# Optimization experiments

Hardware: AMD Instinct MI355X
Metric: run time of the kernel (lower is better)

## Reference

```python
import jax, jax.numpy as jnp
import numpy as np

N, E, DIN, DOUT, DE = 100000, 250000, 32, 32, 13


def setup_inputs() -> dict:
    key = jax.random.key(0)
    ks = jax.random.split(key, 10)
    def u(k, shape, fan):
        b = 1.0 / np.sqrt(fan)
        return jax.random.uniform(k, shape, jnp.float32, -b, b)
    x = jax.random.normal(ks[0], (N, DIN), jnp.float32)
    edge_index = jax.random.randint(ks[1], (2, E), 0, N)
    edge_attr = jax.random.uniform(ks[2], (E, DE), jnp.float32)
    # NNConv's edge network: Linear(DE -> DIN*DOUT)
    nn_w = u(ks[3], (DIN * DOUT, DE), DE)
    nn_b = u(ks[4], (DIN * DOUT,), DE)
    # NNConv root weight + bias
    root = u(ks[5], (DIN, DOUT), DIN)
    bias = jnp.zeros((DOUT,), jnp.float32)
    # GRU(input=DIN, hidden=DOUT), single layer, seq_len=1
    w_ih = u(ks[6], (3 * DOUT, DIN), DOUT)
    w_hh = u(ks[7], (3 * DOUT, DOUT), DOUT)
    b_ih = u(ks[8], (3 * DOUT,), DOUT)
    b_hh = u(ks[9], (3 * DOUT,), DOUT)
    return dict(x=x, edge_attr=edge_attr, nn_w=nn_w, nn_b=nn_b, root=root,
                bias=bias, w_ih=w_ih, w_hh=w_hh, b_ih=b_ih, b_hh=b_hh,
                edge_index=edge_index)


def reference(x, edge_attr, nn_w, nn_b, root, bias, w_ih, w_hh, b_ih, b_hh, edge_index):
    identity = x
    h0 = x  # h is None -> h = x.unsqueeze(0); squeeze the seq dim here
    # norm='_None' (identity) and Dropout in eval mode (identity)
    src, dst = edge_index[0], edge_index[1]
    # NNConv: per-edge weight matrix from edge_attr  [E, DIN, DOUT]
    W = (edge_attr @ nn_w.T + nn_b).reshape(E, DIN, DOUT)
    msg = jnp.einsum('ei,eio->eo', x[src], W)           # [E, DOUT]
    agg = jax.ops.segment_sum(msg, dst, num_segments=N)  # [N, DOUT]
    cnt = jax.ops.segment_sum(jnp.ones((E, 1), x.dtype), dst, num_segments=N)
    mean = agg / jnp.maximum(cnt, 1.0)                   # aggr='mean'
    conv = mean + x @ root + bias
    # celu then GRU step (seq_len=1)
    c = jax.nn.celu(conv)
    gi = c @ w_ih.T + b_ih
    gh = h0 @ w_hh.T + b_hh
    ir, iz, ic = jnp.split(gi, 3, axis=1)
    hr, hz, hc = jnp.split(gh, 3, axis=1)
    r = jax.nn.sigmoid(ir + hr)
    z = jax.nn.sigmoid(iz + hz)
    n = jnp.tanh(ic + r * hc)
    h_new = (1.0 - z) * n + z * h0
    out = jax.nn.relu(h_new + identity)  # res=True, act=ReLU
    return out, h_new[None]
```

## Files before the change

kernel.cpp:

```cpp
#include <hip/hip_runtime.h>
#include <hip/hip_bf16.h>
#include <stdint.h>

#define DIN 32
#define DOUT 32
#define DE 13

typedef float f32x4 __attribute__((ext_vector_type(4)));
typedef short s16x8 __attribute__((ext_vector_type(8)));
typedef int   i32x4 __attribute__((ext_vector_type(4)));

__device__ __forceinline__ float bf2f(unsigned short u) {
    return __uint_as_float(((uint32_t)u) << 16);
}
__device__ __forceinline__ unsigned short f2bf(float f) {
    uint32_t b = __float_as_uint(f);
    b += 0x7FFFu + ((b >> 16) & 1u);
    return (unsigned short)(b >> 16);
}
__device__ __forceinline__ uint32_t pk2(float a, float b) {
    float2 t; t.x = a; t.y = b;
    __hip_bfloat162 h = __float22bfloat162_rn(t);
    return *(uint32_t*)&h;
}
__device__ __forceinline__ float sigm(float v) { return 1.f / (1.f + __expf(-v)); }
__device__ __forceinline__ float tanh_fast(float v) { return 2.f / (1.f + __expf(-2.f * v)) - 1.f; }

#define KE_LDS (28 * 512)
__global__ __launch_bounds__(256) void kE(const float* __restrict__ x,
        const float* __restrict__ ea, const int* __restrict__ ei,
        const float* __restrict__ nn_w, const float* __restrict__ nn_b,
        __hip_bfloat162* __restrict__ agg, float* __restrict__ cnt, int E) {
    __shared__ unsigned short Al[KE_LDS];
    __shared__ uint32_t tr4[4][256];
    const int tid = threadIdx.x;
    for (int t = tid; t < KE_LDS; t += 256) {
        int j = t & 7;
        int lane = (t >> 3) & 63;
        int tile = t >> 9;
        int at2 = tile >= 14 ? 1 : 0;
        int kt = tile - at2 * 14;
        int o = at2 * 16 + (lane & 15);
        int i = ((lane >> 4) << 3) + j;
        float v = (kt < 13) ? nn_w[(i * 32 + o) * 13 + kt] : nn_b[i * 32 + o];
        Al[t] = f2bf(v);
    }
    __syncthreads();
    const int lane = tid & 63;
    const int wv = tid >> 6;
    const int el = lane & 15;
    const int quad = lane >> 4;
    const int q8 = quad << 3;
    uint32_t* trw = &tr4[wv][0];
    const int wave = (blockIdx.x * 256 + tid) >> 6;
    const int nw = (gridDim.x * 256) >> 6;
    const int nstrips = E >> 4;
    for (int s = wave; s < nstrips; s += nw) {
        const int e = (s << 4) + el;
        const int srcv = ei[e];
        const int dstv = ei[E + e];
        const float* eab = ea + (size_t)(s << 4) * 13;
        #pragma unroll
        for (int t = 0; t < 4; ++t) {
            int idx = t * 64 + lane;
            if (idx < 208) trw[idx] = __float_as_uint(eab[idx]);
        }
        const float* xq = x + (size_t)srcv * 32 + q8;
        f32x4 xlo = *(const f32x4*)xq;
        f32x4 xhi = *(const f32x4*)(xq + 4);
        i32x4 bi;
        bi[0] = pk2(xlo[0], xlo[1]);
        bi[1] = pk2(xlo[2], xlo[3]);
        bi[2] = pk2(xhi[0], xhi[1]);
        bi[3] = pk2(xhi[2], xhi[3]);
        s16x8 bfr = __builtin_bit_cast(s16x8, bi);
        float g[14];
        #pragma unroll
        for (int d = 0; d < 13; ++d) g[d] = __uint_as_float(trw[el * 13 + d]);
        g[13] = 1.0f;
        f32x4 acc0 = {0.f, 0.f, 0.f, 0.f}, acc1 = {0.f, 0.f, 0.f, 0.f};
        const f32x4 zz = {0.f, 0.f, 0.f, 0.f};
        #pragma unroll
        for (int kt = 0; kt < 14; ++kt) {
            s16x8 a0 = *(const s16x8*)&Al[kt * 512 + lane * 8];
            s16x8 a1 = *(const s16x8*)&Al[(14 + kt) * 512 + lane * 8];
            f32x4 y0 = __builtin_amdgcn_mfma_f32_16x16x32_bf16(a0, bfr, zz, 0, 0, 0);
            f32x4 y1 = __builtin_amdgcn_mfma_f32_16x16x32_bf16(a1, bfr, zz, 0, 0, 0);
            float gk = g[kt];
            #pragma unroll
            for (int r = 0; r < 4; ++r) {
                acc0[r] = fmaf(gk, y0[r], acc0[r]);
                acc1[r] = fmaf(gk, y1[r], acc1[r]);
            }
        }
        {
            uint2 p0, p1;
            p0.x = pk2(acc0[0], acc0[1]); p0.y = pk2(acc0[2], acc0[3]);
            p1.x = pk2(acc1[0], acc1[1]); p1.y = pk2(acc1[2], acc1[3]);
            *(uint2*)&trw[el * 16 + quad * 2] = p0;
            *(uint2*)&trw[el * 16 + 8 + quad * 2] = p1;
        }
        #pragma unroll
        for (int p = 0; p < 4; ++p) {
            int e4 = (p << 2) + quad;
            uint32_t val = trw[e4 * 16 + el];
            int d4 = __shfl(dstv, e4, 64);
            __hip_bfloat162 hv = *(__hip_bfloat162*)&val;
            unsafeAtomicAdd(&agg[(size_t)d4 * 16 + el], hv);
        }
        if (lane < 16) atomicAdd(&cnt[dstv], 1.0f);
    }
}

__global__ __launch_bounds__(256) void kF(const float* __restrict__ x,
        const __hip_bfloat16* __restrict__ aggb, const float* __restrict__ cnt,
        const float* __restrict__ root, const float* __restrict__ bias,
        const float* __restrict__ w_ih, const float* __restrict__ w_hh,
        const float* __restrict__ b_ih, const float* __restrict__ b_hh,
        float* __restrict__ out, float* __restrict__ hnew, int N) {
    __shared__ __align__(16) char smem[30720];
    unsigned short* Bl = (unsigned short*)smem;
    float* scr = (float*)(smem + 14336);
    unsigned short* clds = (unsigned short*)(smem + 14336);
    const int tid = threadIdx.x;
    {
        *(f32x4*)&scr[tid * 4] = *(const f32x4*)&root[tid * 4];
        #pragma unroll
        for (int it = 0; it < 3; ++it)
            *(f32x4*)&scr[1024 + it * 1024 + tid * 4] =
                *(const f32x4*)&w_ih[0 * 0 + it * 1024 + tid * 4 - 0 * 0] * 0.f +
                *(const f32x4*)&w_hh[it * 1024 + tid * 4];
    }
    __syncthreads();
    for (int t = tid; t < 8 * 512; t += 256) {
        int j = t & 7;
        int ln = (t >> 3) & 63;
        int tt = t >> 9;
        int i = ((ln >> 4) << 3) + j;
        int c = ln & 15;
        int col = tt * 16 + c;
        float v = (col < 32) ? scr[i * 32 + col] : scr[1024 + (col - 32) * 32 + i];
        Bl[t] = f2bf(v);
    }
    __syncthreads();
    #pragma unroll
    for (int it = 0; it < 3; ++it)
        *(f32x4*)&scr[it * 1024 + tid * 4] = *(const f32x4*)&w_ih[it * 1024 + tid * 4];
    __syncthreads();
    for (int t = tid + 8 * 512; t < 14 * 512; t += 256) {
        int j = t & 7;
        int ln = (t >> 3) & 63;
        int tt = t >> 9;
        int i = ((ln >> 4) << 3) + j;
        int c = ln & 15;
        Bl[t] = f2bf(scr[((tt - 8) * 16 + c) * 32 + i]);
    }
    __syncthreads();
    const int lane = tid & 63;
    const int wv = tid >> 6;
    const int c15 = lane & 15;
    const int rowb = (lane >> 4) << 2;
    unsigned short* cl = clds + wv * 512;
    float binit[14];
    #pragma unroll
    for (int t = 0; t < 2; ++t) binit[t] = bias[t * 16 + c15];
    #pragma unroll
    for (int t = 2; t < 8; ++t) binit[t] = b_hh[t * 16 + c15 - 32];
    #pragma unroll
    for (int u = 0; u < 6; ++u) binit[8 + u] = b_ih[u * 16 + c15];
    int wave = (blockIdx.x * 256 + tid) >> 6;
    const int nw = (gridDim.x * 256) >> 6;
    const int nstrips = N >> 4;
    for (int s = wave; s < nstrips; s += nw) {
        const int n0 = s << 4;
        const float* xp = x + (size_t)(n0 + c15) * 32 + ((lane >> 4) << 3);
        f32x4 x0 = *(const f32x4*)xp;
        f32x4 x1 = *(const f32x4*)(xp + 4);
        float xr[4][2], ag[4][2], cn[4];
        #pragma unroll
        for (int r = 0; r < 4; ++r) {
            const int n = n0 + rowb + r;
            cn[r] = cnt[n];
            #pragma unroll
            for (int t = 0; t < 2; ++t) {
                xr[r][t] = x[(size_t)n * 32 + t * 16 + c15];
                ag[r][t] = bf2f(*(const unsigned short*)&aggb[(size_t)n * 32 + t * 16 + c15]);
            }
        }
        s16x8 a;
        a[0] = (short)f2bf(x0[0]); a[1] = (short)f2bf(x0[1]);
        a[2] = (short)f2bf(x0[2]); a[3] = (short)f2bf(x0[3]);
        a[4] = (short)f2bf(x1[0]); a[5] = (short)f2bf(x1[1]);
        a[6] = (short)f2bf(x1[2]); a[7] = (short)f2bf(x1[3]);
        f32x4 D[8];
        #pragma unroll
        for (int t = 0; t < 8; ++t) {
            s16x8 b = *(const s16x8*)&Bl[(t * 64 + lane) * 8];
            f32x4 ci = {binit[t], binit[t], binit[t], binit[t]};
            D[t] = __builtin_amdgcn_mfma_f32_16x16x32_bf16(a, b, ci, 0, 0, 0);
        }
        #pragma unroll
        for (int r = 0; r < 4; ++r) {
            float icn = 1.f / fmaxf(cn[r], 1.f);
            #pragma unroll
            for (int t = 0; t < 2; ++t) {
                float conv = ag[r][t] * icn + D[t][r];
                float cv = conv > 0.f ? conv : (__expf(conv) - 1.f);
                cl[(rowb + r) * 32 + t * 16 + c15] = f2bf(cv);
            }
        }
        s16x8 a2 = *(const s16x8*)&cl[c15 * 32 + ((lane >> 4) << 3)];
        f32x4 G[6];
        #pragma unroll
        for (int u = 0; u < 6; ++u) {
            s16x8 b = *(const s16x8*)&Bl[((8 + u) * 64 + lane) * 8];
            f32x4 ci = {binit[8 + u], binit[8 + u], binit[8 + u], binit[8 + u]};
            G[u] = __builtin_amdgcn_mfma_f32_16x16x32_bf16(a2, b, ci, 0, 0, 0);
        }
        #pragma unroll
        for (int t = 0; t < 2; ++t) {
            #pragma unroll
            for (int r = 0; r < 4; ++r) {
                float rg = sigm(G[t][r] + D[2 + t][r]);
                float z  = sigm(G[2 + t][r] + D[4 + t][r]);
                float nn = tanh_fast(G[4 + t][r] + rg * D[6 + t][r]);
                float h  = (1.f - z) * nn + z * xr[r][t];
                float ov = h + xr[r][t];
                size_t oi = (size_t)(n0 + rowb + r) * 32 + t * 16 + c15;
                out[oi]  = ov > 0.f ? ov : 0.f;
                hnew[oi] = h;
            }
        }
    }
}

extern "C" void kernel_launch(void* const* d_in, const int* in_sizes, int n_in,
                              void* d_out, int out_size, void* d_ws, size_t ws_size,
                              hipStream_t stream) {
    const float* x    = (const float*)d_in[0];
    const float* ea   = (const float*)d_in[1];
    const float* nn_w = (const float*)d_in[2];
    const float* nn_b = (const float*)d_in[3];
    const float* root = (const float*)d_in[4];
    const float* bias = (const float*)d_in[5];
    const float* w_ih = (const float*)d_in[6];
    const float* w_hh = (const float*)d_in[7];
    const float* b_ih = (const float*)d_in[8];
    const float* b_hh = (const float*)d_in[9];
    const int*   ei   = (const int*)d_in[10];
    const int N = in_sizes[0] / DIN;
    const int E = in_sizes[10] / 2;
    float* out  = (float*)d_out;
    float* hnew = out + (size_t)N * DOUT;

    const size_t agg_bytes = (size_t)N * 32 * sizeof(__hip_bfloat16);

    __hip_bfloat162* agg = (__hip_bfloat162*)d_ws;
    float* cnt = (float*)((char*)d_ws + agg_bytes);
    kE<<<1024, 256, 0, stream>>>(x, ea, ei, nn_w, nn_b, agg, cnt, E);
    kF<<<768, 256, 0, stream>>>(x, (const __hip_bfloat16*)d_ws, cnt, root, bias,
                                w_ih, w_hh, b_ih, b_hh, out, hnew, N);
}
```

Baseline: 146.8 us.

## Process 32-edge strips with 32x32x16 MFMA in edge-message kernel

The edge kernel now handles 32 edges per wave using the 32x32x16 bf16 MFMA instead of two 16x16x32 MFMAs per edge-attribute term on 16-edge strips. The LDS weight layout is reorganized to match, and the transpose scratch is padded to a stride of 17 to reduce bank conflicts. Tail handling for edge counts not divisible by 32 is added. This halves the number of strips and aims to raise MFMA efficiency per edge, at the cost of more accumulator registers and extra bounds checks. A dead zero-multiplied w_ih load in kF is also removed.

```diff
diff --git a/kernel.cpp b/kernel.cpp
--- a/kernel.cpp
+++ b/kernel.cpp
@@ -6,9 +6,10 @@
 #define DOUT 32
 #define DE 13
 
-typedef float f32x4 __attribute__((ext_vector_type(4)));
-typedef short s16x8 __attribute__((ext_vector_type(8)));
-typedef int   i32x4 __attribute__((ext_vector_type(4)));
+typedef float f32x4  __attribute__((ext_vector_type(4)));
+typedef float f32x16 __attribute__((ext_vector_type(16)));
+typedef short s16x8  __attribute__((ext_vector_type(8)));
+typedef int   i32x4  __attribute__((ext_vector_type(4)));
 
 __device__ __forceinline__ float bf2f(unsigned short u) {
     return __uint_as_float(((uint32_t)u) << 16);
@@ -32,83 +33,92 @@
         const float* __restrict__ nn_w, const float* __restrict__ nn_b,
         __hip_bfloat162* __restrict__ agg, float* __restrict__ cnt, int E) {
     __shared__ unsigned short Al[KE_LDS];
-    __shared__ uint32_t tr4[4][256];
+    __shared__ uint32_t tr4[4][544];
     const int tid = threadIdx.x;
     for (int t = tid; t < KE_LDS; t += 256) {
         int j = t & 7;
         int lane = (t >> 3) & 63;
         int tile = t >> 9;
-        int at2 = tile >= 14 ? 1 : 0;
-        int kt = tile - at2 * 14;
-        int o = at2 * 16 + (lane & 15);
-        int i = ((lane >> 4) << 3) + j;
-        float v = (kt < 13) ? nn_w[(i * 32 + o) * 13 + kt] : nn_b[i * 32 + o];
+        int d = tile >> 1, half = tile & 1;
+        int o = lane & 31;
+        int k = ((lane >> 5) << 3) + j;
+        int i = half * 16 + k;
+        float v = (d < 13) ? nn_w[(i * 32 + o) * 13 + d] : nn_b[i * 32 + o];
         Al[t] = f2bf(v);
     }
     __syncthreads();
     const int lane = tid & 63;
     const int wv = tid >> 6;
-    const int el = lane & 15;
-    const int quad = lane >> 4;
-    const int q8 = quad << 3;
+    const int el = lane & 31;
+    const int kh = lane >> 5;
     uint32_t* trw = &tr4[wv][0];
     const int wave = (blockIdx.x * 256 + tid) >> 6;
     const int nw = (gridDim.x * 256) >> 6;
-    const int nstrips = E >> 4;
+    const int nstrips = (E + 31) >> 5;
     for (int s = wave; s < nstrips; s += nw) {
-        const int e = (s << 4) + el;
-        const int srcv = ei[e];
-        const int dstv = ei[E + e];
-        const float* eab = ea + (size_t)(s << 4) * 13;
-        #pragma unroll
-        for (int t = 0; t < 4; ++t) {
+        const int e = (s << 5) + el;
+        const bool ev = e < E;
+        const int ec = ev ? e : (E - 1);
+        const int srcv = ei[ec];
+        const int dstv = ei[E + ec];
+        const int ecur = min(32, E - (s << 5));
+        const float* eab = ea + (size_t)(s << 5) * 13;
+        const int lim = ecur * 13;
+        #pragma unroll
+        for (int t = 0; t < 7; ++t) {
             int idx = t * 64 + lane;
-            if (idx < 208) trw[idx] = __float_as_uint(eab[idx]);
-        }
-        const float* xq = x + (size_t)srcv * 32 + q8;
-        f32x4 xlo = *(const f32x4*)xq;
-        f32x4 xhi = *(const f32x4*)(xq + 4);
-        i32x4 bi;
-        bi[0] = pk2(xlo[0], xlo[1]);
-        bi[1] = pk2(xlo[2], xlo[3]);
-        bi[2] = pk2(xhi[0], xhi[1]);
-        bi[3] = pk2(xhi[2], xhi[3]);
-        s16x8 bfr = __builtin_bit_cast(s16x8, bi);
+            if (idx < lim) trw[idx] = __float_as_uint(eab[idx]);
+        }
+        const float* xq = x + (size_t)srcv * 32 + (kh << 3);
+        f32x4 x0a = *(const f32x4*)xq;
+        f32x4 x0b = *(const f32x4*)(xq + 4);
+        f32x4 x1a = *(const f32x4*)(xq + 16);
+        f32x4 x1b = *(const f32x4*)(xq + 20);
+        i32x4 bi0, bi1;
+        bi0[0] = pk2(x0a[0], x0a[1]); bi0[1] = pk2(x0a[2], x0a[3]);
+        bi0[2] = pk2(x0b[0], x0b[1]); bi0[3] = pk2(x0b[2], x0b[3]);
+        bi1[0] = pk2(x1a[0], x1a[1]); bi1[1] = pk2(x1a[2], x1a[3]);
+        bi1[2] = pk2(x1b[0], x1b[1]); bi1[3] = pk2(x1b[2], x1b[3]);
+        s16x8 b0 = __builtin_bit_cast(s16x8, bi0);
+        s16x8 b1 = __builtin_bit_cast(s16x8, bi1);
         float g[14];
         #pragma unroll
         for (int d = 0; d < 13; ++d) g[d] = __uint_as_float(trw[el * 13 + d]);
         g[13] = 1.0f;
-        f32x4 acc0 = {0.f, 0.f, 0.f, 0.f}, acc1 = {0.f, 0.f, 0.f, 0.f};
-        const f32x4 zz = {0.f, 0.f, 0.f, 0.f};
+        float acc[16];
+        #pragma unroll
+        for (int r = 0; r < 16; ++r) acc[r] = 0.f;
+        const f32x16 zz = {0.f,0.f,0.f,0.f,0.f,0.f,0.f,0.f,
+                           0.f,0.f,0.f,0.f,0.f,0.f,0.f,0.f};
         #pragma unroll
         for (int kt = 0; kt < 14; ++kt) {
-            s16x8 a0 = *(const s16x8*)&Al[kt * 512 + lane * 8];
-            s16x8 a1 = *(const s16x8*)&Al[(14 + kt) * 512 + lane * 8];
-            f32x4 y0 = __builtin_amdgcn_mfma_f32_16x16x32_bf16(a0, bfr, zz, 0, 0, 0);
-            f32x4 y1 = __builtin_amdgcn_mfma_f32_16x16x32_bf16(a1, bfr, zz, 0, 0, 0);
+            s16x8 a0 = *(const s16x8*)&Al[(kt * 2) * 512 + lane * 8];
+            s16x8 a1 = *(const s16x8*)&Al[(kt * 2 + 1) * 512 + lane * 8];
+            f32x16 y = __builtin_amdgcn_mfma_f32_32x32x16_bf16(a0, b0, zz, 0, 0, 0);
+            y = __builtin_amdgcn_mfma_f32_32x32x16_bf16(a1, b1, y, 0, 0, 0);
             float gk = g[kt];
             #pragma unroll
-            for (int r = 0; r < 4; ++r) {
-                acc0[r] = fmaf(gk, y0[r], acc0[r]);
-                acc1[r] = fmaf(gk, y1[r], acc1[r]);
-            }
-        }
-        {
-            uint2 p0, p1;
-            p0.x = pk2(acc0[0], acc0[1]); p0.y = pk2(acc0[2], acc0[3]);
-            p1.x = pk2(acc1[0], acc1[1]); p1.y = pk2(acc1[2], acc1[3]);
-            *(uint2*)&trw[el * 16 + quad * 2] = p0;
-            *(uint2*)&trw[el * 16 + 8 + quad * 2] = p1;
-        }
-        #pragma unroll
-        for (int p = 0; p < 4; ++p) {
-            int e4 = (p << 2) + quad;
-            uint32_t val = trw[e4 * 16 + el];
+            for (int r = 0; r < 16; ++r) acc[r] = fmaf(gk, y[r], acc[r]);
+        }
+        #pragma unroll
+        for (int q = 0; q < 4; ++q) {
+            uint2 pr;
+            pr.x = pk2(acc[4 * q], acc[4 * q + 1]);
+            pr.y = pk2(acc[4 * q + 2], acc[4 * q + 3]);
+            *(uint2*)&trw[el * 17 + 4 * q + 2 * kh] = pr;
+        }
+        #pragma unroll
+        for (int p = 0; p < 8; ++p) {
+            int e4 = (p << 2) + (lane >> 4);
+            int pair = lane & 15;
+            uint32_t val = trw[e4 * 17 + pair];
             int d4 = __shfl(dstv, e4, 64);
-            __hip_bfloat162 hv = *(__hip_bfloat162*)&val;
-            unsafeAtomicAdd(&agg[(size_t)d4 * 16 + el], hv);
-        }
-        if (lane < 16) atomicAdd(&cnt[dstv], 1.0f);
+            if ((s << 5) + e4 < E) {
+                __hip_bfloat162 hv = *(__hip_bfloat162*)&val;
+                unsafeAtomicAdd(&agg[(size_t)d4 * 16 + pair], hv);
+            }
+        }
+        if (lane < 32 && ev) atomicAdd(&cnt[dstv], 1.0f);
     }
 }
 
@@ -128,7 +138,6 @@
         #pragma unroll
         for (int it = 0; it < 3; ++it)
             *(f32x4*)&scr[1024 + it * 1024 + tid * 4] =
-                *(const f32x4*)&w_ih[0 * 0 + it * 1024 + tid * 4 - 0 * 0] * 0.f +
                 *(const f32x4*)&w_hh[it * 1024 + tid * 4];
     }
     __syncthreads();
```

New measurement: 176.1 us. 1.2x slower.
